# Kernel tuning notes

Measured on AMD Instinct MI355X. Metric: run time of the kernel, lower is better.

The kernel has to match this reference:

```python
import jax, jax.numpy as jnp
import numpy as np

D_MODEL = 1024
N_HEADS = 16
HEAD_DIM = D_MODEL // N_HEADS
ROPE_BASE = 10000.0


def rotate_half(x):
    d = x.shape[-1]
    x1, x2 = x[..., : d // 2], x[..., d // 2 :]
    return jnp.concatenate((-x2, x1), axis=-1)


def rope_cos_sin(T, dim, dtype):
    inv_freq = 1.0 / (ROPE_BASE ** (jnp.arange(0, dim, 2, dtype=jnp.float32) / dim))
    t = jnp.arange(T, dtype=jnp.float32)
    freqs = jnp.einsum('i,j->ij', t, inv_freq)  # (T, dim//2)
    emb = jnp.concatenate((freqs, freqs), axis=-1)  # (T, dim)
    return jnp.cos(emb).astype(dtype), jnp.sin(emb).astype(dtype)


def setup_inputs() -> dict:
    key = jax.random.key(0)
    ks = jax.random.split(key, 9)
    s = 0.02
    return {
        'x': jax.random.normal(ks[0], (4, 2048, D_MODEL), dtype=jnp.float32),
        'Wq': jax.random.normal(ks[1], (D_MODEL, D_MODEL), dtype=jnp.float32) * s,
        'bq': jax.random.normal(ks[2], (D_MODEL,), dtype=jnp.float32) * s,
        'Wk': jax.random.normal(ks[3], (D_MODEL, D_MODEL), dtype=jnp.float32) * s,
        'bk': jax.random.normal(ks[4], (D_MODEL,), dtype=jnp.float32) * s,
        'Wv': jax.random.normal(ks[5], (D_MODEL, D_MODEL), dtype=jnp.float32) * s,
        'bv': jax.random.normal(ks[6], (D_MODEL,), dtype=jnp.float32) * s,
        'Wo': jax.random.normal(ks[7], (D_MODEL, D_MODEL), dtype=jnp.float32) * s,
        'bo': jax.random.normal(ks[8], (D_MODEL,), dtype=jnp.float32) * s,
    }


def reference(x, Wq, bq, Wk, bk, Wv, bv, Wo, bo):
    B, T, D = x.shape
    H, hd = N_HEADS, HEAD_DIM

    def proj(W, b):
        y = jnp.einsum('btd,ed->bte', x, W) + b  # torch Linear: x @ W.T + b
        return y.reshape(B, T, H, hd).transpose(0, 2, 1, 3)  # (B,H,T,hd)

    q = proj(Wq, bq)
    k = proj(Wk, bk)
    v = proj(Wv, bv)

    cos, sin = rope_cos_sin(T, hd, x.dtype)  # (T, hd)
    q = q * cos + rotate_half(q) * sin
    k = k * cos + rotate_half(k) * sin

    scores = jnp.einsum('bhqd,bhkd->bhqk', q, k) / jnp.sqrt(jnp.asarray(hd, x.dtype))
    causal = jnp.tril(jnp.ones((T, T), dtype=bool))
    scores = jnp.where(causal, scores, jnp.asarray(-jnp.inf, x.dtype))
    attn = jax.nn.softmax(scores, axis=-1)  # dropout=0 (eval)
    out = jnp.einsum('bhqk,bhkd->bhqd', attn, v)
    out = out.transpose(0, 2, 1, 3).reshape(B, T, D)
    return jnp.einsum('btd,ed->bte', out, Wo) + bo
```

## Files before the change

kernel.cpp:

```cpp
#include <hip/hip_runtime.h>
#include <math.h>

typedef unsigned short u16;
typedef unsigned int u32;
typedef __attribute__((ext_vector_type(4))) float f32x4;
typedef __attribute__((ext_vector_type(8))) __bf16 bf16x8;
typedef __attribute__((ext_vector_type(2))) __bf16 bf16x2;
typedef __attribute__((ext_vector_type(2))) u32 u32x2;
typedef __attribute__((ext_vector_type(4))) u32 u32x4;

#define B_ 4
#define T_ 2048
#define D_ 1024
#define H_ 16
#define HD_ 64

__device__ __forceinline__ u16 f2b_rne(float f) {
  u32 u = __float_as_uint(f);
  u32 r = (u + 0x7FFFu + ((u >> 16) & 1u)) >> 16;
  return (u16)r;
}
__device__ __forceinline__ u32 pack2(float a, float b) {
  bf16x2 v = {(__bf16)a, (__bf16)b};
  return __builtin_bit_cast(u32, v);
}
__device__ __forceinline__ void gload_lds16(const void* g, void* l) {
  __builtin_amdgcn_global_load_lds(
      (const __attribute__((address_space(1))) u32*)g,
      (__attribute__((address_space(3))) u32*)l, 16, 0, 0);
}

__global__ void tab_kernel(float2* __restrict__ tab) {
  int idx = blockIdx.x * 256 + threadIdx.x;
  int t = idx >> 5, i = idx & 31;
  float inv_freq = exp2f(-(float)i * 0.4152410118609203f);
  float ang = (float)t * inv_freq;
  float s, c;
  sincosf(ang, &s, &c);
  tab[idx] = make_float2(c, s);
}

__global__ __launch_bounds__(256) void gemm_qkv_kernel(
    const float* __restrict__ X, const float* __restrict__ Wq,
    const float* __restrict__ Wk, const float* __restrict__ Wv,
    const float* __restrict__ bq, const float* __restrict__ bk,
    const float* __restrict__ bv, const float2* __restrict__ tab,
    u16* __restrict__ Q, u16* __restrict__ Kd, u16* __restrict__ VT) {
  __shared__ __align__(16) u16 As[128 * 64];
  __shared__ __align__(16) u16 Bs[128 * 64];
  const int tid = threadIdx.x;
  const int wid = tid >> 6, lane = tid & 63;
  const int l15 = lane & 15, lhi = lane >> 4;
  int lin = blockIdx.y * 64 + blockIdx.x;
  int swz = (lin & 7) * 192 + (lin >> 3);
  const int brow = swz / 24, bcol = swz - brow * 24;
  const int wr = wid >> 1, wc = wid & 1;

  const float* Wm = (bcol < 8) ? Wq : (bcol < 16) ? Wk : Wv;
  const int bcl = bcol & 7;

  f32x4 RA[4][2], RB[4][2];
  auto loadA = [&](int k0) {
#pragma unroll
    for (int p = 0; p < 4; ++p) {
      int s = tid + 256 * p, row = s >> 3, k8 = s & 7;
      const float* ap = X + (size_t)(brow * 128 + row) * 1024 + k0 + k8 * 8;
      RA[p][0] = *(const f32x4*)ap;
      RA[p][1] = *(const f32x4*)(ap + 4);
    }
  };
  auto loadB = [&](int k0) {
#pragma unroll
    for (int p = 0; p < 4; ++p) {
      int s = tid + 256 * p, row = s >> 3, k8 = s & 7;
      const float* bp = Wm + (size_t)(bcl * 128 + row) * 1024 + k0 + k8 * 8;
      RB[p][0] = *(const f32x4*)bp;
      RB[p][1] = *(const f32x4*)(bp + 4);
    }
  };
  auto storeT = [&](u16* dst, f32x4 R[4][2]) {
#pragma unroll
    for (int p = 0; p < 4; ++p) {
      int s = tid + 256 * p, row = s >> 3, k8 = s & 7;
      u32x4 pk;
      pk.x = pack2(R[p][0][0], R[p][0][1]);
      pk.y = pack2(R[p][0][2], R[p][0][3]);
      pk.z = pack2(R[p][1][0], R[p][1][1]);
      pk.w = pack2(R[p][1][2], R[p][1][3]);
      *(u32x4*)&dst[row * 64 + k8 * 8] = pk;
    }
  };

  f32x4 acc[4][4] = {};
  loadA(0);
  loadB(0);
  for (int k0 = 0; k0 < 1024; k0 += 64) {
    __syncthreads();
    storeT(As, RA);
    storeT(Bs, RB);
    if (k0 + 64 < 1024) { loadA(k0 + 64); loadB(k0 + 64); }
    __syncthreads();
#pragma unroll
    for (int kk = 0; kk < 2; kk++) {
      bf16x8 af[4], bfr[4];
#pragma unroll
      for (int i = 0; i < 4; i++)
        af[i] = *(const bf16x8*)&As[(wr * 64 + i * 16 + l15) * 64 + kk * 32 + lhi * 8];
#pragma unroll
      for (int j = 0; j < 4; j++)
        bfr[j] = *(const bf16x8*)&Bs[(wc * 64 + j * 16 + l15) * 64 + kk * 32 + lhi * 8];
#pragma unroll
      for (int i = 0; i < 4; i++)
#pragma unroll
        for (int j = 0; j < 4; j++)
          acc[i][j] = __builtin_amdgcn_mfma_f32_16x16x32_bf16(af[i], bfr[j], acc[i][j], 0, 0, 0);
    }
  }

  const int b = brow >> 4;
  const int tb0 = (brow & 15) * 128 + wr * 64;
  if (bcol < 16) {
    const bool isQ = bcol < 8;
    const float* bias = isQ ? bq : bk;
    u16* dst0 = isQ ? Q : Kd;
    const int h = (bcol & 7) * 2 + wc;
    const float scl = isQ ? 0.18033688011f : 1.0f;
#pragma unroll
    for (int i = 0; i < 4; ++i)
#pragma unroll
      for (int r = 0; r < 4; ++r) {
        int t = tb0 + i * 16 + lhi * 4 + r;
#pragma unroll
        for (int j = 0; j < 2; ++j) {
          int ii = j * 16 + l15;
          float v1 = acc[i][j][r] + bias[h * 64 + ii];
          float v2 = acc[i][j + 2][r] + bias[h * 64 + ii + 32];
          float2 cs = tab[t * 32 + ii];
          float o1 = (v1 * cs.x - v2 * cs.y) * scl;
          float o2 = (v2 * cs.x + v1 * cs.y) * scl;
          u16* dp = dst0 + ((size_t)(b * 16 + h) * 2048 + t) * 64 + ii;
          dp[0] = f2b_rne(o1);
          dp[32] = f2b_rne(o2);
        }
      }
  } else {
    const int h = (bcol - 16) * 2 + wc;
#pragma unroll
    for (int i = 0; i < 4; ++i)
#pragma unroll
      for (int r = 0; r < 4; ++r) {
        int t = tb0 + i * 16 + lhi * 4 + r;
#pragma unroll
        for (int j = 0; j < 4; ++j) {
          int ii = j * 16 + l15;
          float v = acc[i][j][r] + bv[h * 64 + ii];
          VT[((size_t)(b * 16 + h) * 64 + ii) * 2048 + t] = f2b_rne(v);
        }
      }
  }
}

__global__ __launch_bounds__(256) void attn_kernel(
    const u16* __restrict__ Q, const u16* __restrict__ K,
    const u16* __restrict__ VT, u16* __restrict__ O) {
  __shared__ __align__(16) u16 Plds[4][2][16 * 64];
  const int tid = threadIdx.x;
  const int w = tid >> 6, lane = tid & 63;
  const int l15 = lane & 15, lhi = lane >> 4;
  const int xcd = blockIdx.x & 7;
  const int head = (blockIdx.x >> 3) & 7;
  const int qt = 15 - (blockIdx.x >> 6);
  const int bh = (xcd << 3) | head;
  const int qbase = qt * 128 + w * 32;
  const int bb = bh >> 4, hh = bh & 15;

  const u16* Qb = Q + (size_t)bh * T_ * HD_;
  const u16* Kb = K + (size_t)bh * T_ * HD_;
  const u16* Vb = VT + (size_t)bh * HD_ * T_;
  const int sw = (l15 & 7) << 4;
  const float CMAX = 16.f;

  const int qrw[2] = {qbase + l15, qbase + 16 + l15};

  bf16x8 qf[2][2];
#pragma unroll
  for (int g = 0; g < 2; ++g) {
    const u16* qr = Qb + (size_t)qrw[g] * HD_ + lhi * 8;
    qf[g][0] = *(const bf16x8*)(qr);
    qf[g][1] = *(const bf16x8*)(qr + 32);
  }

  float lp[2] = {0.f, 0.f};
  f32x4 oacc[2][4] = {};

  const int nb = (qbase + 95) >> 6;

  for (int t = 0; t < nb; ++t) {
    const int t0 = t * 64;

    bf16x8 kf[8];
#pragma unroll
    for (int ks = 0; ks < 4; ++ks) {
      const u16* kr = Kb + (size_t)(t0 + ks * 16 + l15) * HD_ + lhi * 8;
      kf[ks * 2] = *(const bf16x8*)(kr);
      kf[ks * 2 + 1] = *(const bf16x8*)(kr + 32);
    }
    f32x4 s[2][4];
    __builtin_amdgcn_s_setprio(1);
#pragma unroll
    for (int ks = 0; ks < 4; ++ks)
#pragma unroll
      for (int g = 0; g < 2; ++g) {
        f32x4 z = {0.f, 0.f, 0.f, 0.f};
        z = __builtin_amdgcn_mfma_f32_16x16x32_bf16(kf[ks * 2], qf[g][0], z, 0, 0, 0);
        s[g][ks] = __builtin_amdgcn_mfma_f32_16x16x32_bf16(kf[ks * 2 + 1], qf[g][1], z, 0, 0, 0);
      }
    __builtin_amdgcn_s_setprio(0);

    bf16x8 vf[8];
#pragma unroll
    for (int db = 0; db < 4; ++db) {
      const u16* vr = Vb + (size_t)(db * 16 + l15) * T_ + t0 + lhi * 8;
      vf[db * 2] = *(const bf16x8*)(vr);
      vf[db * 2 + 1] = *(const bf16x8*)(vr + 32);
    }

    if (t == nb - 1) {
#pragma unroll
      for (int g = 0; g < 2; ++g)
#pragma unroll
        for (int ks = 0; ks < 4; ++ks)
#pragma unroll
          for (int r = 0; r < 4; ++r)
            if (t0 + ks * 16 + lhi * 4 + r > qrw[g]) s[g][ks][r] = -1e30f;
    }

#pragma unroll
    for (int g = 0; g < 2; ++g) {
      char* prow = (char*)&Plds[w][g][0] + l15 * 128;
      float rsp = 0.f;
#pragma unroll
      for (int ks = 0; ks < 4; ++ks) {
        float e0 = exp2f(s[g][ks][0] - CMAX);
        float e1 = exp2f(s[g][ks][1] - CMAX);
        float e2 = exp2f(s[g][ks][2] - CMAX);
        float e3 = exp2f(s[g][ks][3] - CMAX);
        rsp += (e0 + e1) + (e2 + e3);
        u32x2 pw;
        pw.x = pack2(e0, e1);
        pw.y = pack2(e2, e3);
        *(u32x2*)(prow + ((ks * 32 + lhi * 8) ^ sw)) = pw;
      }
      lp[g] += rsp;
    }

    __builtin_amdgcn_s_setprio(1);
#pragma unroll
    for (int g = 0; g < 2; ++g) {
      const char* prow = (const char*)&Plds[w][g][0] + l15 * 128;
#pragma unroll
      for (int c = 0; c < 2; ++c) {
        bf16x8 pb = *(const bf16x8*)(prow + ((c * 64 + lhi * 16) ^ sw));
#pragma unroll
        for (int db = 0; db < 4; ++db)
          oacc[g][db] = __builtin_amdgcn_mfma_f32_16x16x32_bf16(vf[db * 2 + c], pb, oacc[g][db], 0, 0, 0);
      }
    }
    __builtin_amdgcn_s_setprio(0);
  }

#pragma unroll
  for (int g = 0; g < 2; ++g) {
    float l = lp[g];
    l += __shfl_xor(l, 16);
    l += __shfl_xor(l, 32);
    float invl = 1.0f / l;
    u16* orow = O + ((size_t)bb * T_ + qrw[g]) * D_ + hh * HD_ + lhi * 4;
#pragma unroll
    for (int db = 0; db < 4; ++db) {
      u32x2 wv;
      wv.x = pack2(oacc[g][db][0] * invl, oacc[g][db][1] * invl);
      wv.y = pack2(oacc[g][db][2] * invl, oacc[g][db][3] * invl);
      *(u32x2*)(orow + db * 16) = wv;
    }
  }
}

__global__ __launch_bounds__(256) void gemm_out_kernel(
    const u16* __restrict__ A, const float* __restrict__ Wo,
    const float* __restrict__ bo, float* __restrict__ Cout) {
  __shared__ __align__(16) u16 As[128 * 64];
  __shared__ __align__(16) u16 Bs[128 * 64];
  const int tid = threadIdx.x;
  const int wid = tid >> 6, lane = tid & 63;
  const int l15 = lane & 15, lhi = lane >> 4;
  int lin = blockIdx.y * 64 + blockIdx.x;
  int swz = (lin & 7) * 64 + (lin >> 3);
  const int brow = swz / 8, bcol = swz - brow * 8;
  const int wr = wid >> 1, wc = wid & 1;

  f32x4 RB[4][2];
  auto loadB = [&](int k0) {
#pragma unroll
    for (int p = 0; p < 4; ++p) {
      int s = tid + 256 * p, row = s >> 3, k8 = s & 7;
      const float* bp = Wo + (size_t)(bcol * 128 + row) * 1024 + k0 + k8 * 8;
      RB[p][0] = *(const f32x4*)bp;
      RB[p][1] = *(const f32x4*)(bp + 4);
    }
  };

  f32x4 acc[4][4] = {};
  loadB(0);
  for (int k0 = 0; k0 < 1024; k0 += 64) {
    __syncthreads();
#pragma unroll
    for (int p = 0; p < 4; ++p) {
      int s = tid + 256 * p, row = s >> 3, k8 = s & 7;
      u32x4 pk;
      pk.x = pack2(RB[p][0][0], RB[p][0][1]);
      pk.y = pack2(RB[p][0][2], RB[p][0][3]);
      pk.z = pack2(RB[p][1][0], RB[p][1][1]);
      pk.w = pack2(RB[p][1][2], RB[p][1][3]);
      *(u32x4*)&Bs[row * 64 + k8 * 8] = pk;
    }
#pragma unroll
    for (int cc = 0; cc < 4; cc++) {
      int chunk = cc * 4 + wid;
      int slot = chunk * 64 + lane;
      int row = slot >> 3;
      int colb = (slot & 7) << 4;
      gload_lds16((const char*)(A + (size_t)(brow * 128 + row) * 1024 + k0) + colb,
                  (char*)As + chunk * 1024);
    }
    if (k0 + 64 < 1024) loadB(k0 + 64);
    __syncthreads();
#pragma unroll
    for (int kk = 0; kk < 2; kk++) {
      bf16x8 af[4], bfr[4];
#pragma unroll
      for (int i = 0; i < 4; i++)
        af[i] = *(const bf16x8*)&As[(wr * 64 + i * 16 + l15) * 64 + kk * 32 + lhi * 8];
#pragma unroll
      for (int j = 0; j < 4; j++)
        bfr[j] = *(const bf16x8*)&Bs[(wc * 64 + j * 16 + l15) * 64 + kk * 32 + lhi * 8];
#pragma unroll
      for (int i = 0; i < 4; i++)
#pragma unroll
        for (int j = 0; j < 4; j++)
          acc[i][j] = __builtin_amdgcn_mfma_f32_16x16x32_bf16(af[i], bfr[j], acc[i][j], 0, 0, 0);
    }
  }
#pragma unroll
  for (int i = 0; i < 4; i++)
#pragma unroll
    for (int r = 0; r < 4; r++) {
      int row = brow * 128 + wr * 64 + i * 16 + lhi * 4 + r;
#pragma unroll
      for (int j = 0; j < 4; j++) {
        int col = bcol * 128 + wc * 64 + j * 16 + l15;
        Cout[(size_t)row * 1024 + col] = acc[i][j][r] + bo[col];
      }
    }
}

extern "C" void kernel_launch(void* const* d_in, const int* in_sizes, int n_in,
                              void* d_out, int out_size, void* d_ws, size_t ws_size,
                              hipStream_t stream) {
  const float* x  = (const float*)d_in[0];
  const float* Wq = (const float*)d_in[1];
  const float* bq = (const float*)d_in[2];
  const float* Wk = (const float*)d_in[3];
  const float* bk = (const float*)d_in[4];
  const float* Wv = (const float*)d_in[5];
  const float* bv = (const float*)d_in[6];
  const float* Wo = (const float*)d_in[7];
  const float* bo = (const float*)d_in[8];

  char* ws = (char*)d_ws;
  u16*    Qb   = (u16*)(ws + 0);
  u16*    Kb   = (u16*)(ws + 16777216);
  u16*    VTb  = (u16*)(ws + 33554432);
  u16*    ATTO = (u16*)(ws + 50331648);
  float2* TAB  = (float2*)(ws + 67108864);

  tab_kernel<<<256, 256, 0, stream>>>(TAB);

  gemm_qkv_kernel<<<dim3(64, 24), 256, 0, stream>>>(
      x, Wq, Wk, Wv, bq, bk, bv, TAB, Qb, Kb, VTb);

  attn_kernel<<<1024, 256, 0, stream>>>(Qb, Kb, VTb, ATTO);

  gemm_out_kernel<<<dim3(64, 8), 256, 0, stream>>>(ATTO, Wo, bo, (float*)d_out);

  (void)in_sizes; (void)n_in; (void)out_size; (void)ws_size;
}
```

Measured before the change: 286.6 us.

## Pre-convert X to bf16 with direct LDS loads; split attention into single-wave blocks

Adds a pass that converts x to bf16 once, then the QKV GEMM loads the A tile straight into LDS with global_load_lds instead of loading fp32 into registers and converting it again in each of the 24 column blocks. Separately, the attention kernel is restructured from 256-thread blocks covering 128 queries into 64-thread single-wave blocks covering 32 queries each, with 4096 blocks. This is meant to cut redundant A-side conversion and global traffic and to give finer-grained scheduling for the causal load imbalance. The cost is an extra kernel launch plus a 16MB bf16 write and read.

```diff
diff --git a/kernel.cpp b/kernel.cpp
--- a/kernel.cpp
+++ b/kernel.cpp
@@ -40,8 +40,19 @@
   tab[idx] = make_float2(c, s);
 }
 
+__global__ void f2b4_kernel(const float* __restrict__ in, u16* __restrict__ out, int n4) {
+  int i = blockIdx.x * 256 + threadIdx.x;
+  if (i < n4) {
+    f32x4 v = ((const f32x4*)in)[i];
+    u32x2 o;
+    o.x = pack2(v[0], v[1]);
+    o.y = pack2(v[2], v[3]);
+    ((u32x2*)out)[i] = o;
+  }
+}
+
 __global__ __launch_bounds__(256) void gemm_qkv_kernel(
-    const float* __restrict__ X, const float* __restrict__ Wq,
+    const u16* __restrict__ XB, const float* __restrict__ Wq,
     const float* __restrict__ Wk, const float* __restrict__ Wv,
     const float* __restrict__ bq, const float* __restrict__ bk,
     const float* __restrict__ bv, const float2* __restrict__ tab,
@@ -59,16 +70,7 @@
   const float* Wm = (bcol < 8) ? Wq : (bcol < 16) ? Wk : Wv;
   const int bcl = bcol & 7;
 
-  f32x4 RA[4][2], RB[4][2];
-  auto loadA = [&](int k0) {
-#pragma unroll
-    for (int p = 0; p < 4; ++p) {
-      int s = tid + 256 * p, row = s >> 3, k8 = s & 7;
-      const float* ap = X + (size_t)(brow * 128 + row) * 1024 + k0 + k8 * 8;
-      RA[p][0] = *(const f32x4*)ap;
-      RA[p][1] = *(const f32x4*)(ap + 4);
-    }
-  };
+  f32x4 RB[4][2];
   auto loadB = [&](int k0) {
 #pragma unroll
     for (int p = 0; p < 4; ++p) {
@@ -78,27 +80,31 @@
       RB[p][1] = *(const f32x4*)(bp + 4);
     }
   };
-  auto storeT = [&](u16* dst, f32x4 R[4][2]) {
+
+  f32x4 acc[4][4] = {};
+  loadB(0);
+  for (int k0 = 0; k0 < 1024; k0 += 64) {
+    __syncthreads();
 #pragma unroll
     for (int p = 0; p < 4; ++p) {
       int s = tid + 256 * p, row = s >> 3, k8 = s & 7;
       u32x4 pk;
-      pk.x = pack2(R[p][0][0], R[p][0][1]);
-      pk.y = pack2(R[p][0][2], R[p][0][3]);
-      pk.z = pack2(R[p][1][0], R[p][1][1]);
-      pk.w = pack2(R[p][1][2], R[p][1][3]);
-      *(u32x4*)&dst[row * 64 + k8 * 8] = pk;
-    }
-  };
-
-  f32x4 acc[4][4] = {};
-  loadA(0);
-  loadB(0);
-  for (int k0 = 0; k0 < 1024; k0 += 64) {
-    __syncthreads();
-    storeT(As, RA);
-    storeT(Bs, RB);
-    if (k0 + 64 < 1024) { loadA(k0 + 64); loadB(k0 + 64); }
+      pk.x = pack2(RB[p][0][0], RB[p][0][1]);
+      pk.y = pack2(RB[p][0][2], RB[p][0][3]);
+      pk.z = pack2(RB[p][1][0], RB[p][1][1]);
+      pk.w = pack2(RB[p][1][2], RB[p][1][3]);
+      *(u32x4*)&Bs[row * 64 + k8 * 8] = pk;
+    }
+#pragma unroll
+    for (int cc = 0; cc < 4; cc++) {
+      int chunk = cc * 4 + wid;
+      int slot = chunk * 64 + lane;
+      int row = slot >> 3;
+      int colb = (slot & 7) << 4;
+      gload_lds16((const char*)(XB + (size_t)(brow * 128 + row) * 1024 + k0) + colb,
+                  (char*)As + chunk * 1024);
+    }
+    if (k0 + 64 < 1024) loadB(k0 + 64);
     __syncthreads();
 #pragma unroll
     for (int kk = 0; kk < 2; kk++) {
@@ -160,18 +166,16 @@
   }
 }
 
-__global__ __launch_bounds__(256) void attn_kernel(
+__global__ void attn_kernel(
     const u16* __restrict__ Q, const u16* __restrict__ K,
     const u16* __restrict__ VT, u16* __restrict__ O) {
-  __shared__ __align__(16) u16 Plds[4][2][16 * 64];
-  const int tid = threadIdx.x;
-  const int w = tid >> 6, lane = tid & 63;
+  __shared__ __align__(16) u16 Plds[2][16 * 64];
+  const int lane = threadIdx.x;
   const int l15 = lane & 15, lhi = lane >> 4;
-  const int xcd = blockIdx.x & 7;
-  const int head = (blockIdx.x >> 3) & 7;
-  const int qt = 15 - (blockIdx.x >> 6);
-  const int bh = (xcd << 3) | head;
-  const int qbase = qt * 128 + w * 32;
+  const int bid = blockIdx.x;
+  const int a = 63 - (bid >> 6);
+  const int bh = ((bid & 7) << 3) | ((bid >> 3) & 7);
+  const int qbase = a * 32;
   const int bb = bh >> 4, hh = bh & 15;
 
   const u16* Qb = Q + (size_t)bh * T_ * HD_;
@@ -237,7 +241,7 @@
 
 #pragma unroll
     for (int g = 0; g < 2; ++g) {
-      char* prow = (char*)&Plds[w][g][0] + l15 * 128;
+      char* prow = (char*)&Plds[g][0] + l15 * 128;
       float rsp = 0.f;
 #pragma unroll
       for (int ks = 0; ks < 4; ++ks) {
@@ -257,7 +261,7 @@
     __builtin_amdgcn_s_setprio(1);
 #pragma unroll
     for (int g = 0; g < 2; ++g) {
-      const char* prow = (const char*)&Plds[w][g][0] + l15 * 128;
+      const char* prow = (const char*)&Plds[g][0] + l15 * 128;
 #pragma unroll
       for (int c = 0; c < 2; ++c) {
         bf16x8 pb = *(const bf16x8*)(prow + ((c * 64 + lhi * 16) ^ sw));
@@ -378,18 +382,20 @@
   const float* bo = (const float*)d_in[8];
 
   char* ws = (char*)d_ws;
-  u16*    Qb   = (u16*)(ws + 0);
-  u16*    Kb   = (u16*)(ws + 16777216);
-  u16*    VTb  = (u16*)(ws + 33554432);
-  u16*    ATTO = (u16*)(ws + 50331648);
-  float2* TAB  = (float2*)(ws + 67108864);
+  u16*    XB   = (u16*)(ws + 0);
+  u16*    Qb   = (u16*)(ws + 16777216);
+  u16*    Kb   = (u16*)(ws + 33554432);
+  u16*    VTb  = (u16*)(ws + 50331648);
+  u16*    ATTO = (u16*)(ws + 67108864);
+  float2* TAB  = (float2*)(ws + 83886080);
 
   tab_kernel<<<256, 256, 0, stream>>>(TAB);
+  f2b4_kernel<<<8192, 256, 0, stream>>>(x, XB, B_ * T_ * D_ / 4);
 
   gemm_qkv_kernel<<<dim3(64, 24), 256, 0, stream>>>(
-      x, Wq, Wk, Wv, bq, bk, bv, TAB, Qb, Kb, VTb);
-
-  attn_kernel<<<1024, 256, 0, stream>>>(Qb, Kb, VTb, ATTO);
+      XB, Wq, Wk, Wv, bq, bk, bv, TAB, Qb, Kb, VTb);
+
+  attn_kernel<<<4096, 64, 0, stream>>>(Qb, Kb, VTb, ATTO);
 
   gemm_out_kernel<<<dim3(64, 8), 256, 0, stream>>>(ATTO, Wo, bo, (float*)d_out);
 
```

Result: slower. 354.5 us (+23.7%).
